# Kernel tuning notes

Hardware: AMD Instinct MI355X
Metric: run time of the kernel (lower is better)

## Reference

```python
import jax, jax.numpy as jnp
import numpy as np
import math

# ---- module config (mirrors init_kwargs) ----
FRAME_H, FRAME_W = 480, 640
HFOV = 79.0
CAM_H_CM = 88.0            # camera_height * 100
NUM_SEM = 16
RES = 5                    # map_resolution (cm/cell)
MAP_SIZE_CM = 4800
DSC = 4                    # global_downscaling
DU = 4                     # du_scale
VR = 100                   # vision_range (cells)
CAT_THR, EXP_THR, MAP_THR = 5.0, 1.0, 1.0
MIN_D_CM, MAX_D_CM = 50.0, 350.0
NC = 6                     # MC.NON_SEM_CHANNELS
ML = MAP_SIZE_CM // DSC // RES   # 240 local map cells
MG = MAP_SIZE_CM // RES          # 960 global map cells
ZMIN = int(-40 / RES)            # -8
ZB = int(360 / RES) - ZMIN       # 80 z bins
MIN_MAP_H = int(25 / RES - ZMIN)            # 13
MAX_MAP_H = int((CAM_H_CM + 1) / RES - ZMIN)  # 25
BC_R = 200 // RES                # been-close radius (cells)
CENTER_POSE = (ML * RES) / 200.0 # agent start at local map center (m)


def _affine_grid(theta, H, W):
    # theta: (B,2,3); align_corners=True convention
    ys = jnp.linspace(-1.0, 1.0, H)
    xs = jnp.linspace(-1.0, 1.0, W)
    xg, yg = jnp.meshgrid(xs, ys)
    base = jnp.stack([xg, yg, jnp.ones_like(xg)], -1)  # (H,W,3)
    return jnp.einsum('bij,hwj->bhwi', theta, base)    # (B,H,W,2)


def _grid_sample(img, grid):
    # bilinear, align_corners=True, zero padding (matches F.grid_sample)
    B, C, H, W = img.shape
    x = (grid[..., 0] + 1.0) * 0.5 * (W - 1)
    y = (grid[..., 1] + 1.0) * 0.5 * (H - 1)
    x0, y0 = jnp.floor(x), jnp.floor(y)
    flat = img.reshape(B, C, H * W)
    out = jnp.zeros_like(img)
    for dx in (0.0, 1.0):
        for dy in (0.0, 1.0):
            xi, yi = x0 + dx, y0 + dy
            w = (1.0 - jnp.abs(x - xi)) * (1.0 - jnp.abs(y - yi))
            ok = (xi >= 0) & (xi <= W - 1) & (yi >= 0) & (yi <= H - 1)
            idx = (jnp.clip(yi, 0, H - 1).astype(jnp.int32) * W
                   + jnp.clip(xi, 0, W - 1).astype(jnp.int32))
            g = jnp.take_along_axis(flat, jnp.broadcast_to(idx.reshape(B, 1, -1), (B, C, H * W)), axis=2)
            out = out + g.reshape(B, C, H, W) * (w * ok)[:, None]
    return out


def _splat(gx, gy, gz, feat, valid):
    # trilinear scatter-add of per-point features into (VR,VR,ZB) voxel grid
    # gx,gy,gz,valid: (B,P); feat: (B,P,F)
    B, P = gx.shape
    F = feat.shape[-1]
    ncell = VR * VR * ZB
    acc = jnp.zeros((B * ncell, F), feat.dtype)
    base = (jnp.arange(B) * ncell)[:, None]
    x0, y0, z0 = jnp.floor(gx), jnp.floor(gy), jnp.floor(gz)
    for dx in (0.0, 1.0):
        for dy in (0.0, 1.0):
            for dz in (0.0, 1.0):
                xi, yi, zi = x0 + dx, y0 + dy, z0 + dz
                w = (1.0 - jnp.abs(gx - xi)) * (1.0 - jnp.abs(gy - yi)) * (1.0 - jnp.abs(gz - zi))
                ok = valid & (xi >= 0) & (xi < VR) & (yi >= 0) & (yi < VR) & (zi >= 0) & (zi < ZB)
                cell = (yi.astype(jnp.int32) * VR + xi.astype(jnp.int32)) * ZB + zi.astype(jnp.int32)
                idx = jnp.clip(base + cell, 0, B * ncell - 1).reshape(-1)
                upd = (feat * (w * ok.astype(feat.dtype))[..., None]).reshape(B * P, F)
                acc = acc.at[idx].add(upd)
    return acc.reshape(B, VR, VR, ZB, F).transpose(0, 4, 1, 2, 3)  # (B,F,VR,VR,ZB)


def _forward(seq_obs, seq_pose_delta, seq_camera_poses, init_local_map,
             init_global_map, init_local_pose, init_global_pose,
             init_lmb, init_origins, seq_dones, seq_update_global):
    B, T = seq_obs.shape[:2]
    C = NUM_SEM
    f = FRAME_W / (2.0 * math.tan(math.radians(HFOV) / 2.0))
    cx, cy = FRAME_W / 2.0, FRAME_H / 2.0
    xs = ((jnp.arange(0, FRAME_W, DU) - cx) / f).astype(jnp.float32)   # (Ws,)
    zr = ((cy - jnp.arange(0, FRAME_H, DU)) / f).astype(jnp.float32)   # (Hs,)
    # camera tilt (elevation) from extrinsics (identity -> 0)
    elev = jnp.arctan2(seq_camera_poses[:, 2, 1], seq_camera_poses[:, 2, 2])
    ce, se = jnp.cos(elev)[:, None, None], jnp.sin(elev)[:, None, None]
    Hs, Ws = FRAME_H // DU, FRAME_W // DU
    P = Hs * Ws
    row = jnp.arange(ML, dtype=jnp.float32)

    def step(carry, inp):
        local_map, global_map, pose = carry
        obs, pd, done, upd = inp
        done = done.astype(bool)
        upd = upd.astype(bool)
        # episode reset
        local_map = jnp.where(done[:, None, None, None], 0.0, local_map)
        global_map = jnp.where(done[:, None, None, None], 0.0, global_map)
        pose = jnp.where(done[:, None], jnp.array([CENTER_POSE, CENTER_POSE, 0.0], jnp.float32), pose)
        # pose update (get_new_pose_batch, degrees)
        tr = jnp.radians(pose[:, 2])
        nx = pose[:, 0] + pd[:, 0] * jnp.cos(tr) - pd[:, 1] * jnp.sin(tr)
        ny = pose[:, 1] + pd[:, 0] * jnp.sin(tr) + pd[:, 1] * jnp.cos(tr)
        nt = jnp.mod(pose[:, 2] + jnp.degrees(pd[:, 2]) + 180.0, 360.0) - 180.0
        pose = jnp.stack([nx, ny, nt], -1)
        # ---- depth -> egocentric point cloud (cm) ----
        d = obs[:, 3, ::DU, ::DU]                           # (B,Hs,Ws)
        valid = (d >= MIN_D_CM) & (d <= MAX_D_CM)
        lat = d * xs[None, None, :]
        up = d * zr[None, :, None]
        fwd = d * ce + up * se
        hgt = -d * se + up * ce + CAM_H_CM
        gx = (lat / RES + VR / 2.0).reshape(B, P)
        gy = (fwd / RES).reshape(B, P)
        gz = (hgt / RES - ZMIN).reshape(B, P)
        # features: occupancy + avg-pooled semantics (du_scale pooling)
        sem = obs[:, 4:].reshape(B, C, Hs, DU, Ws, DU).mean((3, 5))
        feat = jnp.concatenate([jnp.ones((B, 1, Hs, Ws), obs.dtype), sem], 1)
        feat = feat.reshape(B, 1 + C, P).transpose(0, 2, 1)  # (B,P,F)
        vox = _splat(gx, gy, gz, feat, valid.reshape(B, P))  # (B,F,VR,VR,ZB)
        agent_hp = vox[..., MIN_MAP_H:MAX_MAP_H].sum(-1)
        all_hp = vox.sum(-1)
        fp_map = jnp.clip(agent_hp[:, 0:1] / MAP_THR, 0.0, 1.0)
        fp_exp = jnp.clip(all_hp[:, 0:1] / EXP_THR, 0.0, 1.0)
        sem_pred = jnp.clip(agent_hp[:, 1:] / CAT_THR, 0.0, 1.0)
        agent_view = jnp.zeros((B, NC + C, ML, ML), obs.dtype)
        y1, x1 = ML // 2, ML // 2 - VR // 2
        agent_view = agent_view.at[:, 0:1, y1:y1 + VR, x1:x1 + VR].set(fp_map)
        agent_view = agent_view.at[:, 1:2, y1:y1 + VR, x1:x1 + VR].set(fp_exp)
        agent_view = agent_view.at[:, NC:, y1:y1 + VR, x1:x1 + VR].set(sem_pred)
        # ---- pose transform: rotation then translation grid_sample ----
        th = jnp.radians(90.0 - pose[:, 2])
        stx = -(pose[:, 0] * 100.0 / RES - ML / 2.0) / (ML / 2.0)
        sty = -(pose[:, 1] * 100.0 / RES - ML / 2.0) / (ML / 2.0)
        c, s = jnp.cos(th), jnp.sin(th)
        z0 = jnp.zeros_like(th)
        o1 = jnp.ones_like(th)
        th_rot = jnp.stack([jnp.stack([c, -s, z0], -1), jnp.stack([s, c, z0], -1)], 1)
        th_tr = jnp.stack([jnp.stack([o1, z0, stx], -1), jnp.stack([z0, o1, sty], -1)], 1)
        warped = _grid_sample(_grid_sample(agent_view, _affine_grid(th_rot, ML, ML)),
                              _affine_grid(th_tr, ML, ML))
        # dilate obstacle channel (3x3 ones kernel, 1 iter)
        obst = jax.lax.reduce_window(warped[:, 0:1], -jnp.inf, jax.lax.max,
                                     (1, 1, 3, 3), (1, 1, 1, 1), 'SAME')
        warped = warped.at[:, 0:1].set(obst)
        local_map = jnp.maximum(local_map, warped)
        # current location / visited / been-close disks
        acx, acy = pose[:, 0] * 100.0 / RES, pose[:, 1] * 100.0 / RES
        d2 = ((row[None, None, :] - acx[:, None, None]) ** 2
              + (row[None, :, None] - acy[:, None, None]) ** 2)
        curr = (d2 <= 4.0).astype(local_map.dtype)
        local_map = local_map.at[:, 2].set(curr)
        local_map = local_map.at[:, 3].max(curr)
        local_map = local_map.at[:, 4].max((d2 <= float(BC_R ** 2)).astype(local_map.dtype))
        # global map update at local map boundaries
        gnew = jax.vmap(lambda g, l, lm: jax.lax.dynamic_update_slice(g, l, (0, lm[0], lm[2])))(
            global_map, local_map, init_lmb)
        global_map = jnp.where(upd[:, None, None, None], gnew, global_map)
        gpose = pose + init_origins
        # map features: local NC ch + maxpooled global NC ch + local sem ch
        gmax = global_map[:, :NC].reshape(B, NC, MG // DSC, DSC, MG // DSC, DSC).max((3, 5))
        mf = jnp.concatenate([local_map[:, :NC], gmax, local_map[:, NC:]], 1)
        return (local_map, global_map, pose), (mf, pose, gpose)

    xs_t = (jnp.swapaxes(seq_obs, 0, 1), jnp.swapaxes(seq_pose_delta, 0, 1),
            jnp.swapaxes(seq_dones, 0, 1), jnp.swapaxes(seq_update_global, 0, 1))
    (fl, fg, _), (mfs, lps, gps) = jax.lax.scan(
        step, (init_local_map, init_global_map, init_local_pose), xs_t)
    seq_mf = jnp.swapaxes(mfs, 0, 1)
    seq_lp = jnp.swapaxes(lps, 0, 1)
    seq_gp = jnp.swapaxes(gps, 0, 1)
    seq_lmb = jnp.broadcast_to(init_lmb[:, None], (B, T, 4))
    seq_org = jnp.broadcast_to(init_origins[:, None], (B, T, 3))
    return seq_mf, fl, fg, seq_lp, seq_gp, seq_lmb, seq_org


def setup_inputs():
    key = jax.random.key(0)
    k0, k1 = jax.random.split(key)
    B, T = 4, 4
    obs = jax.random.uniform(k0, (B, T, 4 + NUM_SEM, FRAME_H, FRAME_W), jnp.float32)
    obs = obs.at[:, :, 3].set(MIN_D_CM + obs[:, :, 3] * (MAX_D_CM - MIN_D_CM))  # depth in cm
    obs = obs.at[:, :, 4:].set((obs[:, :, 4:] > 0.9).astype(jnp.float32))       # binary seg masks
    pd = jax.random.normal(k1, (B, T, 3), jnp.float32) * jnp.array([0.25, 0.05, 0.1], jnp.float32)
    lo = (MG - ML) // 2
    lmb = jnp.tile(jnp.array([[lo, lo + ML, lo, lo + ML]], jnp.int32), (B, 1))
    origins = jnp.concatenate([jnp.full((B, 2), lo * RES / 100.0, jnp.float32),
                               jnp.zeros((B, 1), jnp.float32)], 1)
    lp = jnp.concatenate([jnp.full((B, 2), CENTER_POSE, jnp.float32),
                          jnp.zeros((B, 1), jnp.float32)], 1)
    return {
        "seq_obs": obs,
        "seq_pose_delta": pd,
        "seq_camera_poses": jnp.broadcast_to(jnp.eye(4, dtype=jnp.float32), (B, 4, 4)),
        "init_local_map": jnp.zeros((B, NC + NUM_SEM, ML, ML), jnp.float32),
        "init_global_map": jnp.zeros((B, NC + NUM_SEM, MG, MG), jnp.float32),
        "init_local_pose": lp,
        "init_global_pose": lp + origins,
        "init_origins": origins,
        "seq_dones": jnp.zeros((B, T), jnp.int32),
        "seq_update_global": jnp.ones((B, T), jnp.int32),
        "init_lmb": lmb,
    }


def reference(seq_obs, seq_pose_delta, seq_camera_poses, init_local_map, init_global_map,
              init_local_pose, init_global_pose, init_origins, seq_dones,
              seq_update_global, init_lmb):
    return _forward(seq_obs, seq_pose_delta, seq_camera_poses, init_local_map,
                    init_global_map, init_local_pose, init_global_pose,
                    init_lmb, init_origins, seq_dones, seq_update_global)
```

## Files before the change

kernel.cpp:

```cpp
#include <hip/hip_runtime.h>
#include <math.h>

#ifndef M_PI
#define M_PI 3.14159265358979323846
#endif

#define BB 4
#define TT 4
#define NSEM 16
#define CHL 22
#define CHMF 28
#define ML 240
#define MG 960
#define VR 100
#define HS 120
#define WSW 160
#define NPL 18
#define CPAD 24
#define MLSQ (ML*ML)
#define MGSQ (MG*MG)
#define VRSQ (VR*VR)
#define PPT (HS*WSW)
#define NPART 12
#define PR 9
#define NGRP 5

#define SZ_MF (BB*TT*CHMF*MLSQ)
#define SZ_FL (BB*CHL*MLSQ)
#define SZ_FG (BB*CHL*MGSQ)
#define OFF_FL SZ_MF
#define OFF_FG (OFF_FL + SZ_FL)
#define OFF_LP (OFF_FG + SZ_FG)
#define OFF_GP (OFF_LP + BB*TT*3)
#define OFF_LMB (OFF_GP + BB*TT*3)
#define OFF_ORG (OFF_LMB + BB*TT*4)

#define WS_SCAL 0
#define WS_FLAGS (WS_SCAL + BB*TT*8)
#define WS_CACHE (WS_FLAGS + 4*BB)
#define WS_PLANES (WS_CACHE + BB*6*MLSQ)
#define WS_I2 (WS_PLANES + BB*TT*VRSQ*CPAD)
#define PTSN (BB*TT*PPT)
#define WS_GY (WS_I2 + BB*TT*NPL*MLSQ)
#define WS_GX (WS_GY + PTSN)
#define WS_WZA (WS_GX + PTSN)
#define WS_WZL (WS_WZA + PTSN)
#define WS_SEMDS (WS_WZL + PTSN)

__global__ __launch_bounds__(256) void k_stage1(const float* __restrict__ obs,
                                                const float* __restrict__ cam,
                                                const float* __restrict__ pd,
                                                const float* __restrict__ ilp,
                                                const float* __restrict__ org,
                                                const int* __restrict__ lmb,
                                                const int* __restrict__ dones,
                                                const int* __restrict__ updg,
                                                float* __restrict__ out,
                                                float* __restrict__ ws)
{
    if (blockIdx.x == 0) {
        int i = threadIdx.x;
        if (i < BB*TT) {
            int b = i / TT, t = i % TT;
            for (int k = 0; k < 4; k++) out[OFF_LMB + (b*TT+t)*4 + k] = (float)lmb[b*4+k];
            for (int k = 0; k < 3; k++) out[OFF_ORG + (b*TT+t)*3 + k] = org[b*3+k];
        }
        if (i >= BB) return;
        int b = i;
        float p0 = ilp[b*3+0], p1 = ilp[b*3+1], p2 = ilp[b*3+2];
        const float D2R = 0.017453292519943295f;
        int lastDone = -1, lastUpd = -1;
        for (int t = 0; t < TT; t++) {
            if (dones[b*TT+t]) { p0 = 6.0f; p1 = 6.0f; p2 = 0.0f; lastDone = t; }
            if (updg[b*TT+t]) lastUpd = t;
            float tr = p2 * D2R;
            float c0 = cosf(tr), s0 = sinf(tr);
            float q0 = pd[(b*TT+t)*3+0], q1 = pd[(b*TT+t)*3+1], q2 = pd[(b*TT+t)*3+2];
            float nx = p0 + q0*c0 - q1*s0;
            float ny = p1 + q0*s0 + q1*c0;
            float a  = p2 + q2*57.29577951308232f + 180.0f;
            float m  = fmodf(a, 360.0f); if (m < 0.0f) m += 360.0f;
            float nt = m - 180.0f;
            p0 = nx; p1 = ny; p2 = nt;
            out[OFF_LP + (b*TT+t)*3+0] = nx;
            out[OFF_LP + (b*TT+t)*3+1] = ny;
            out[OFF_LP + (b*TT+t)*3+2] = nt;
            out[OFF_GP + (b*TT+t)*3+0] = nx + org[b*3+0];
            out[OFF_GP + (b*TT+t)*3+1] = ny + org[b*3+1];
            out[OFF_GP + (b*TT+t)*3+2] = nt + org[b*3+2];
            float th = (90.0f - nt) * D2R;
            float ax = nx*100.0f/5.0f, ay = ny*100.0f/5.0f;
            float* sc = ws + WS_SCAL + (b*TT+t)*8;
            sc[0] = cosf(th);
            sc[1] = sinf(th);
            sc[2] = -(ax - 120.0f)/120.0f;
            sc[3] = -(ay - 120.0f)/120.0f;
            sc[4] = ax;
            sc[5] = ay;
        }
        ws[WS_FLAGS + b*4 + 0] = (lastDone >= 0) ? 1.0f : 0.0f;
        ws[WS_FLAGS + b*4 + 1] = (lastUpd < lastDone) ? 1.0f : 0.0f;
        ws[WS_FLAGS + b*4 + 2] = (float)lastUpd;
        return;
    }
    int bb = blockIdx.x - 1;
    int bt = bb / 75;
    int b = bt / TT;
    int p = (bb % 75)*256 + threadIdx.x;
    int h = p / WSW, w = p % WSW;
    size_t pi = (size_t)bt*PPT + p;
    const float* ob = obs + (size_t)bt * 20 * 480 * 640;
    float d = ob[(size_t)(3*480 + 4*h)*640 + 4*w];
    if (!(d >= 50.0f && d <= 350.0f)) { ws[WS_GY + pi] = -1000.0f; return; }

    double fd = 640.0 / (2.0 * tan((79.0 * M_PI / 180.0) * 0.5));
    float ff  = (float)fd;
    float xsv = (float)(4*w - 320) / ff;
    float zrv = (240.0f - (float)(4*h)) / ff;
    float elev = atan2f(cam[b*16+9], cam[b*16+10]);
    float ce = cosf(elev), se = sinf(elev);
    float up  = d * zrv;
    float fwd = d*ce + up*se;
    float hgt = -d*se + up*ce + 88.0f;
    float gx = (d*xsv)/5.0f + 50.0f;
    float gy = fwd/5.0f;
    float gz = hgt/5.0f + 8.0f;

    float z0 = floorf(gz);
    float wza = 0.0f, wzl = 0.0f;
    #pragma unroll
    for (int dz = 0; dz < 2; dz++) {
        float zi = z0 + dz;
        float wz = 1.0f - fabsf(gz - zi);
        if (zi >= 0.0f && zi < 80.0f) {
            wzl += wz;
            if (zi >= 13.0f && zi < 25.0f) wza += wz;
        }
    }
    if (wzl == 0.0f && wza == 0.0f) { ws[WS_GY + pi] = -1000.0f; return; }

    ws[WS_GY + pi]  = gy;
    ws[WS_GX + pi]  = gx;
    ws[WS_WZA + pi] = wza;
    ws[WS_WZL + pi] = wzl;

    if (wza > 0.0f) {
        const float* sb = ob + (size_t)4*480*640 + (size_t)(4*h)*640 + 4*w;
        float* so = ws + WS_SEMDS + (size_t)bt*NSEM*PPT + p;
        #pragma unroll
        for (int k = 0; k < NSEM; k++) {
            float s = 0.0f;
            #pragma unroll
            for (int r = 0; r < 4; r++) {
                const float4 v = *(const float4*)(sb + (size_t)k*480*640 + r*640);
                s += v.x + v.y + v.z + v.w;
            }
            so[(size_t)k*PPT] = s * 0.0625f;
        }
    }
}

__global__ __launch_bounds__(256) void k_splat2(const float* __restrict__ ws,
                                                float* __restrict__ planes)
{
    int bt = blockIdx.x;
    int part = blockIdx.y;
    int grp = blockIdx.z;
    int rlo = part * PR;
    int c0  = (grp == 0) ? 0 : (2 + 4*(grp-1));
    int nch = (grp == 0) ? 2 : 4;
    __shared__ float acc[4*PR*VR];
    for (int e = threadIdx.x; e < nch*PR*VR; e += 256) acc[e] = 0.0f;
    __syncthreads();

    const float* gyA  = ws + WS_GY  + (size_t)bt*PPT;
    const float* gxA  = ws + WS_GX  + (size_t)bt*PPT;
    const float* wzaA = ws + WS_WZA + (size_t)bt*PPT;
    const float* wzlA = ws + WS_WZL + (size_t)bt*PPT;
    const float* semA = ws + WS_SEMDS + (size_t)bt*NSEM*PPT + (size_t)(c0-2)*PPT;

    for (int p = threadIdx.x; p < PPT; p += 256) {
        float gy = gyA[p];
        float y0 = floorf(gy);
        if (y0 > (float)(rlo + PR - 1) || y0 + 1.0f < (float)rlo) continue;
        float wza = wzaA[p];
        if (grp != 0 && wza <= 0.0f) continue;
        float gx  = gxA[p];
        float x0 = floorf(gx);
        float sem[4];
        if (grp != 0) {
            #pragma unroll
            for (int k = 0; k < 4; k++) sem[k] = semA[(size_t)k*PPT + p];
        }
        float wzl = (grp == 0) ? wzlA[p] : 0.0f;
        #pragma unroll
        for (int dy = 0; dy < 2; dy++) {
            float yi = y0 + dy;
            if (!(yi >= 0.0f && yi < 100.0f)) continue;
            int r = (int)yi - rlo;
            if (r < 0 || r >= PR) continue;
            float wy = 1.0f - fabsf(gy - yi);
            #pragma unroll
            for (int dx = 0; dx < 2; dx++) {
                float xi = x0 + dx;
                if (!(xi >= 0.0f && xi < 100.0f)) continue;
                float wxy = (1.0f - fabsf(gx - xi)) * wy;
                if (wxy <= 0.0f) continue;
                int cell = r*VR + (int)xi;
                if (grp == 0) {
                    if (wza > 0.0f) atomicAdd(&acc[cell], wza*wxy);
                    if (wzl > 0.0f) atomicAdd(&acc[PR*VR + cell], wzl*wxy);
                } else {
                    #pragma unroll
                    for (int k = 0; k < 4; k++) {
                        float sv = sem[k];
                        if (sv != 0.0f) atomicAdd(&acc[k*PR*VR + cell], sv*wza*wxy);
                    }
                }
            }
        }
    }
    __syncthreads();

    int nrows = 100 - rlo; if (nrows > PR) nrows = PR;
    if (nrows <= 0) return;
    float* pl = planes + (size_t)bt*VRSQ*CPAD;
    for (int e = threadIdx.x; e < nch*nrows*VR; e += 256) {
        int c = e / (nrows*VR);
        int rc = e % (nrows*VR);
        int r = rc / VR, x = rc % VR;
        pl[(size_t)((rlo + r)*VR + x)*CPAD + (c0 + c)] = acc[c*PR*VR + r*VR + x];
    }
}

__global__ __launch_bounds__(256) void k_stage3(const float* __restrict__ planes,
                                                const float* __restrict__ igm,
                                                const int* __restrict__ dones,
                                                const int* __restrict__ lmb,
                                                float* __restrict__ I2,
                                                float* __restrict__ fg,
                                                float* __restrict__ out,
                                                float* __restrict__ ws)
{
    int bid = blockIdx.x;
    if (bid < 3600) {
        int bt = bid / 225;
        int idx = (bid % 225)*256 + threadIdx.x;
        int i = idx / ML, j = idx % ML;
        const float* sc = ws + WS_SCAL + bt*8;
        float c = sc[0], s = sc[1], stx = sc[2], sty = sc[3];
        float* o = I2 + (size_t)bt*NPL*MLSQ + idx;
        const float* pl = planes + (size_t)bt*VRSQ*CPAD;

        int   soff[16];
        float sw[16];
        float wsum = 0.0f;
        {
            float xg = (float)j * (float)(2.0/239.0) - 1.0f + stx;
            float yg = (float)i * (float)(2.0/239.0) - 1.0f + sty;
            float x = (xg + 1.0f)*0.5f*239.0f;
            float y = (yg + 1.0f)*0.5f*239.0f;
            float x0 = floorf(x), y0 = floorf(y);
            #pragma unroll
            for (int dy = 0; dy < 2; dy++) {
                float yi = y0 + dy;
                bool vy = (yi >= 0.0f && yi <= 239.0f);
                float wy = 1.0f - fabsf(y - yi);
                #pragma unroll
                for (int dx = 0; dx < 2; dx++) {
                    float xi = x0 + dx;
                    bool vx = (xi >= 0.0f && xi <= 239.0f);
                    float w2v = (vy && vx) ? (1.0f - fabsf(x - xi)) * wy : 0.0f;
                    int ci = (dy*2 + dx)*4;
                    float xg1 = (float)(int)xi * (float)(2.0/239.0) - 1.0f;
                    float yg1 = (float)(int)yi * (float)(2.0/239.0) - 1.0f;
                    float gxr = c*xg1 - s*yg1;
                    float gyr = s*xg1 + c*yg1;
                    float xx = (gxr + 1.0f)*0.5f*239.0f;
                    float yy = (gyr + 1.0f)*0.5f*239.0f;
                    float xx0 = floorf(xx), yy0 = floorf(yy);
                    #pragma unroll
                    for (int dy1 = 0; dy1 < 2; dy1++) {
                        float syi = yy0 + dy1;
                        bool v1y = (syi >= 120.0f && syi < 220.0f);
                        float wy1 = 1.0f - fabsf(yy - syi);
                        #pragma unroll
                        for (int dx1 = 0; dx1 < 2; dx1++) {
                            float sxi = xx0 + dx1;
                            bool v1 = v1y && (sxi >= 70.0f && sxi < 170.0f);
                            float w1v = v1 ? (1.0f - fabsf(xx - sxi)) * wy1 : 0.0f;
                            float wt = w2v * w1v;
                            soff[ci + dy1*2 + dx1] = v1 ? ((int)syi - 120)*VR + ((int)sxi - 70) : 0;
                            sw[ci + dy1*2 + dx1] = wt;
                            wsum += wt;
                        }
                    }
                }
            }
        }

        if (wsum <= 0.0f) {
            #pragma unroll
            for (int cc = 0; cc < NPL; cc++) o[(size_t)cc*MLSQ] = 0.0f;
            return;
        }
        float acc[NPL];
        #pragma unroll
        for (int cc = 0; cc < NPL; cc++) acc[cc] = 0.0f;
        #pragma unroll
        for (int k = 0; k < 16; k++) {
            float w = sw[k];
            if (w == 0.0f) continue;
            const float* pb = pl + (size_t)soff[k]*CPAD;
            float4 a0 = *(const float4*)(pb + 0);
            float4 a1 = *(const float4*)(pb + 4);
            float4 a2 = *(const float4*)(pb + 8);
            float4 a3 = *(const float4*)(pb + 12);
            float2 a4 = *(const float2*)(pb + 16);
            acc[0]  += fminf(a0.x, 1.0f) * w;
            acc[1]  += fminf(a0.y, 1.0f) * w;
            acc[2]  += fminf(a0.z / 5.0f, 1.0f) * w;
            acc[3]  += fminf(a0.w / 5.0f, 1.0f) * w;
            acc[4]  += fminf(a1.x / 5.0f, 1.0f) * w;
            acc[5]  += fminf(a1.y / 5.0f, 1.0f) * w;
            acc[6]  += fminf(a1.z / 5.0f, 1.0f) * w;
            acc[7]  += fminf(a1.w / 5.0f, 1.0f) * w;
            acc[8]  += fminf(a2.x / 5.0f, 1.0f) * w;
            acc[9]  += fminf(a2.y / 5.0f, 1.0f) * w;
            acc[10] += fminf(a2.z / 5.0f, 1.0f) * w;
            acc[11] += fminf(a2.w / 5.0f, 1.0f) * w;
            acc[12] += fminf(a3.x / 5.0f, 1.0f) * w;
            acc[13] += fminf(a3.y / 5.0f, 1.0f) * w;
            acc[14] += fminf(a3.z / 5.0f, 1.0f) * w;
            acc[15] += fminf(a3.w / 5.0f, 1.0f) * w;
            acc[16] += fminf(a4.x / 5.0f, 1.0f) * w;
            acc[17] += fminf(a4.y / 5.0f, 1.0f) * w;
        }
        #pragma unroll
        for (int cc = 0; cc < NPL; cc++) o[(size_t)cc*MLSQ] = acc[cc];
        return;
    }
    int fb = bid - 3600;
    int blk = fb % 225;
    int c = (fb / 225) % CHL;
    int b = fb / (225*CHL);
    int idx = blk*256 + threadIdx.x;
    int i = idx / ML, j = idx % ML;
    bool anyDone = ws[WS_FLAGS + b*4 + 0] > 0.5f;
    bool zeroWin = ws[WS_FLAGS + b*4 + 1] > 0.5f;
    int lastUpd  = (int)ws[WS_FLAGS + b*4 + 2];
    int y0 = lmb[b*4+0], x0 = lmb[b*4+2];
    int iy0 = y0 >> 2, ix0 = x0 >> 2;
    bool inWin = (i >= iy0) && (i < iy0 + ML/4) && (j >= ix0) && (j < ix0 + ML/4);

    size_t base = ((size_t)b*CHL + c)*MGSQ + (size_t)(4*i)*MG + 4*j;
    const float* g = igm + base;
    float* go = fg + base;

    int act;
    if (inWin) act = zeroWin ? 1 : ((lastUpd >= 0) ? 2 : (anyDone ? 1 : 0));
    else       act = anyDone ? 1 : 0;

    if (c < 6) {
        float m = -3.0e38f;
        #pragma unroll
        for (int r = 0; r < 4; r++) {
            float4 q = *(const float4*)(g + (size_t)r*MG);
            if (act == 0) *(float4*)(go + (size_t)r*MG) = q;
            else if (act == 1) *(float4*)(go + (size_t)r*MG) = make_float4(0,0,0,0);
            m = fmaxf(m, fmaxf(fmaxf(q.x, q.y), fmaxf(q.z, q.w)));
        }
        ws[WS_CACHE + ((size_t)b*6 + c)*MLSQ + idx] = m;
        if (!inWin) {
            float v = m;
            for (int t = 0; t < TT; t++) {
                if (dones[b*TT+t]) v = 0.0f;
                out[(size_t)(b*TT+t)*CHMF*MLSQ + (6+c)*MLSQ + idx] = v;
            }
        }
    } else {
        if (act == 2) return;
        if (act == 1) {
            float4 z = make_float4(0,0,0,0);
            #pragma unroll
            for (int r = 0; r < 4; r++) *(float4*)(go + (size_t)r*MG) = z;
        } else {
            #pragma unroll
            for (int r = 0; r < 4; r++)
                *(float4*)(go + (size_t)r*MG) = *(const float4*)(g + (size_t)r*MG);
        }
    }
}

__global__ __launch_bounds__(256) void k_updl7(const float* __restrict__ I2,
                                               const float* __restrict__ ws,
                                               const float* __restrict__ ilm,
                                               const int* __restrict__ dones,
                                               const int* __restrict__ updg,
                                               const int* __restrict__ lmb,
                                               float* __restrict__ fl,
                                               float* __restrict__ fg,
                                               float* __restrict__ out)
{
    int bz = blockIdx.z;
    int b = bz / 7, g = bz % 7;
    int gi = blockIdx.y;
    int bx = blockIdx.x;
    int lane = threadIdx.x & 63, wv = threadIdx.x >> 6;
    int j0 = (bx < 3) ? bx*64 : 176;
    int j = j0 + lane;
    int i = gi*4 + wv;
    int idx = i*ML + j;

    int ncl, cl[4];
    switch (g) {
        case 0:  ncl = 1; cl[0] = 0; cl[1] = 0; cl[2] = 0; cl[3] = 0; break;
        case 1:  ncl = 3; cl[0] = 1; cl[1] = 2; cl[2] = 3; cl[3] = 0; break;
        case 2:  ncl = 2; cl[0] = 4; cl[1] = 5; cl[2] = 0; cl[3] = 0; break;
        default: ncl = 4; { int cc0 = 6 + (g-3)*4;
                 cl[0] = cc0; cl[1] = cc0+1; cl[2] = cc0+2; cl[3] = cc0+3; } break;
    }
    bool hasG = (g <= 2);

    __shared__ float red[4][3][16];

    const float* lmsrc = ilm + (size_t)b*CHL*MLSQ;
    float* lm = fl + (size_t)b*CHL*MLSQ;
    int y0 = lmb[b*4+0], x0 = lmb[b*4+2];
    bool zeroWin = ws[WS_FLAGS + b*4 + 1] > 0.5f;
    int lastUpd = (int)ws[WS_FLAGS + b*4 + 2];

    float S[4];
    #pragma unroll
    for (int q = 0; q < 4; q++) {
        int c = cl[q];
        S[q] = (q < ncl && c != 2) ? lmsrc[c*MLSQ + idx] : 0.0f;
    }

    bool writer = hasG && (wv == 0) && ((lane & 3) == 0);
    int cx = lane >> 2;
    int cellY = (y0 >> 2) + gi;
    int cellX = (x0 >> 2) + (j0 >> 2) + cx;
    float W[3];
    if (writer) {
        #pragma unroll
        for (int q = 0; q < 3; q++)
            if (q < ncl)
                W[q] = ws[WS_CACHE + ((size_t)b*6 + cl[q])*MLSQ + cellY*ML + cellX];
    }

    for (int t = 0; t < TT; t++) {
        int bt = b*TT + t;
        bool done = dones[bt] != 0;
        bool upd  = updg[bt] != 0;
        const float* src = I2 + (size_t)bt*NPL*MLSQ;
        float* mf = out + (size_t)bt*CHMF*MLSQ;

        float pooled = -3.0e38f;
        if (g == 0) {
            for (int di = -1; di <= 1; di++) {
                int ii = i + di; if (ii < 0 || ii >= ML) continue;
                for (int dj = -1; dj <= 1; dj++) {
                    int jj = j + dj; if (jj < 0 || jj >= ML) continue;
                    pooled = fmaxf(pooled, src[ii*ML + jj]);
                }
            }
        }
        const float* sc = ws + WS_SCAL + bt*8;
        float acx = sc[4], acy = sc[5];
        float ddx = (float)j - acx, ddy = (float)i - acy;
        float d2 = ddx*ddx + ddy*ddy;
        float curr = (d2 <= 4.0f) ? 1.0f : 0.0f;
        float bc   = (d2 <= 1600.0f) ? 1.0f : 0.0f;

        size_t goff = (size_t)(y0+i)*MG + (x0+j);
        bool wrG = (t == lastUpd) && !zeroWin;

        #pragma unroll
        for (int q = 0; q < 4; q++) {
            if (q >= ncl) continue;
            int c = cl[q];
            if (done) S[q] = 0.0f;
            float nv;
            if      (c == 0) nv = fmaxf(S[q], pooled);
            else if (c == 1) nv = fmaxf(S[q], src[MLSQ + idx]);
            else if (c == 2) nv = curr;
            else if (c == 3) nv = fmaxf(S[q], curr);
            else if (c == 4) nv = fmaxf(S[q], bc);
            else if (c == 5) nv = S[q];
            else             nv = fmaxf(S[q], src[(size_t)(c-4)*MLSQ + idx]);
            S[q] = nv;
            mf[(size_t)(c < 6 ? c : c + 6)*MLSQ + idx] = nv;
            if (wrG) fg[((size_t)b*CHL + c)*MGSQ + goff] = nv;
        }

        if (hasG) {
            #pragma unroll
            for (int q = 0; q < 3; q++) {
                if (q >= ncl) continue;
                float v = S[q];
                v = fmaxf(v, __shfl_xor(v, 1, 64));
                v = fmaxf(v, __shfl_xor(v, 2, 64));
                if ((lane & 3) == 0) red[wv][q][cx] = v;
            }
            __syncthreads();
            if (writer) {
                #pragma unroll
                for (int q = 0; q < 3; q++) {
                    if (q >= ncl) continue;
                    if (done) W[q] = 0.0f;
                    if (upd)  W[q] = fmaxf(fmaxf(red[0][q][cx], red[1][q][cx]),
                                           fmaxf(red[2][q][cx], red[3][q][cx]));
                    mf[(size_t)(6 + cl[q])*MLSQ + cellY*ML + cellX] = W[q];
                }
            }
            __syncthreads();
        }
    }
    #pragma unroll
    for (int q = 0; q < 4; q++)
        if (q < ncl) lm[(size_t)cl[q]*MLSQ + idx] = S[q];
}

extern "C" void kernel_launch(void* const* d_in, const int* in_sizes, int n_in,
                              void* d_out, int out_size, void* d_ws, size_t ws_size,
                              hipStream_t stream)
{
    const float* obs   = (const float*)d_in[0];
    const float* pd    = (const float*)d_in[1];
    const float* cam   = (const float*)d_in[2];
    const float* ilm   = (const float*)d_in[3];
    const float* igm   = (const float*)d_in[4];
    const float* ilp   = (const float*)d_in[5];
    const float* org   = (const float*)d_in[7];
    const int*   dones = (const int*)d_in[8];
    const int*   updg  = (const int*)d_in[9];
    const int*   lmb   = (const int*)d_in[10];
    float* out = (float*)d_out;
    float* ws  = (float*)d_ws;

    float* fl     = out + OFF_FL;
    float* fg     = out + OFF_FG;
    float* planes = ws + WS_PLANES;
    float* I2v    = ws + WS_I2;

    k_stage1<<<1 + 75*BB*TT, 256, 0, stream>>>(obs, cam, pd, ilp, org, lmb,
                                               dones, updg, out, ws);
    k_splat2<<<dim3(BB*TT, NPART, NGRP), 256, 0, stream>>>(ws, planes);
    k_stage3<<<3600 + 225*CHL*BB, 256, 0, stream>>>(planes, igm, dones, lmb,
                                                    I2v, fg, out, ws);
    k_updl7<<<dim3(4, 60, BB*7), 256, 0, stream>>>(I2v, ws, ilm, dones, updg, lmb,
                                                   fl, fg, out);
}
```

Measured before the change: 358.4 us.

## Spread global-map init work across the first three kernels to overlap stages

The global-map initialisation (downsample max, copy or zero of 22 channels) used to run entirely in the third kernel. It is now split across the first three kernels: channels 0-5 alongside the point projection, 6-13 alongside the splat, and 14-21 alongside the plane processing. Each piece computes its done/update flags locally instead of reading them from the workspace. The aim is to fill idle CUs during the small projection and splat launches with bandwidth-heavy copy work, at the cost of larger grids and mixed block types in each kernel.

```diff
diff --git a/kernel.cpp b/kernel.cpp
--- a/kernel.cpp
+++ b/kernel.cpp
@@ -24,6 +24,7 @@
 #define NPART 12
 #define PR 9
 #define NGRP 5
+#define NSPLAT (BB*TT*NPART*NGRP)
 
 #define SZ_MF (BB*TT*CHMF*MLSQ)
 #define SZ_FL (BB*CHL*MLSQ)
@@ -47,16 +48,79 @@
 #define WS_WZL (WS_WZA + PTSN)
 #define WS_SEMDS (WS_WZL + PTSN)
 
-__global__ __launch_bounds__(256) void k_stage1(const float* __restrict__ obs,
-                                                const float* __restrict__ cam,
-                                                const float* __restrict__ pd,
-                                                const float* __restrict__ ilp,
-                                                const float* __restrict__ org,
-                                                const int* __restrict__ lmb,
-                                                const int* __restrict__ dones,
-                                                const int* __restrict__ updg,
-                                                float* __restrict__ out,
-                                                float* __restrict__ ws)
+__device__ __forceinline__ void fginit_block(const float* __restrict__ igm,
+                                             const int* __restrict__ dones,
+                                             const int* __restrict__ updg,
+                                             const int* __restrict__ lmb,
+                                             float* __restrict__ fg,
+                                             float* __restrict__ out,
+                                             float* __restrict__ ws,
+                                             int b, int c, int idx)
+{
+    int i = idx / ML, j = idx % ML;
+    int lastDone = -1, lastUpd = -1;
+    #pragma unroll
+    for (int t = 0; t < TT; t++) {
+        if (dones[b*TT+t]) lastDone = t;
+        if (updg[b*TT+t])  lastUpd  = t;
+    }
+    bool anyDone = lastDone >= 0;
+    bool zeroWin = lastUpd < lastDone;
+    int y0 = lmb[b*4+0], x0 = lmb[b*4+2];
+    int iy0 = y0 >> 2, ix0 = x0 >> 2;
+    bool inWin = (i >= iy0) && (i < iy0 + ML/4) && (j >= ix0) && (j < ix0 + ML/4);
+
+    size_t base = ((size_t)b*CHL + c)*MGSQ + (size_t)(4*i)*MG + 4*j;
+    const float* g = igm + base;
+    float* go = fg + base;
+
+    int act;
+    if (inWin) act = zeroWin ? 1 : ((lastUpd >= 0) ? 2 : (anyDone ? 1 : 0));
+    else       act = anyDone ? 1 : 0;
+
+    if (c < 6) {
+        float m = -3.0e38f;
+        #pragma unroll
+        for (int r = 0; r < 4; r++) {
+            float4 q = *(const float4*)(g + (size_t)r*MG);
+            if (act == 0) *(float4*)(go + (size_t)r*MG) = q;
+            else if (act == 1) *(float4*)(go + (size_t)r*MG) = make_float4(0,0,0,0);
+            m = fmaxf(m, fmaxf(fmaxf(q.x, q.y), fmaxf(q.z, q.w)));
+        }
+        ws[WS_CACHE + ((size_t)b*6 + c)*MLSQ + idx] = m;
+        if (!inWin) {
+            float v = m;
+            for (int t = 0; t < TT; t++) {
+                if (dones[b*TT+t]) v = 0.0f;
+                out[(size_t)(b*TT+t)*CHMF*MLSQ + (6+c)*MLSQ + idx] = v;
+            }
+        }
+    } else {
+        if (act == 2) return;
+        if (act == 1) {
+            float4 z = make_float4(0,0,0,0);
+            #pragma unroll
+            for (int r = 0; r < 4; r++) *(float4*)(go + (size_t)r*MG) = z;
+        } else {
+            #pragma unroll
+            for (int r = 0; r < 4; r++)
+                *(float4*)(go + (size_t)r*MG) = *(const float4*)(g + (size_t)r*MG);
+        }
+    }
+}
+
+__global__ __launch_bounds__(256) void k_node1(const float* __restrict__ obs,
+                                               const float* __restrict__ cam,
+                                               const float* __restrict__ pd,
+                                               const float* __restrict__ ilp,
+                                               const float* __restrict__ org,
+                                               const int* __restrict__ lmb,
+                                               const int* __restrict__ dones,
+                                               const int* __restrict__ updg,
+                                               const float* __restrict__ igm,
+                                               float* __restrict__ fg,
+                                               float* __restrict__ out,
+                                               float* __restrict__ ws)
 {
     if (blockIdx.x == 0) {
         int i = threadIdx.x;
@@ -103,144 +167,168 @@
         ws[WS_FLAGS + b*4 + 2] = (float)lastUpd;
         return;
     }
-    int bb = blockIdx.x - 1;
-    int bt = bb / 75;
-    int b = bt / TT;
-    int p = (bb % 75)*256 + threadIdx.x;
-    int h = p / WSW, w = p % WSW;
-    size_t pi = (size_t)bt*PPT + p;
-    const float* ob = obs + (size_t)bt * 20 * 480 * 640;
-    float d = ob[(size_t)(3*480 + 4*h)*640 + 4*w];
-    if (!(d >= 50.0f && d <= 350.0f)) { ws[WS_GY + pi] = -1000.0f; return; }
-
-    double fd = 640.0 / (2.0 * tan((79.0 * M_PI / 180.0) * 0.5));
-    float ff  = (float)fd;
-    float xsv = (float)(4*w - 320) / ff;
-    float zrv = (240.0f - (float)(4*h)) / ff;
-    float elev = atan2f(cam[b*16+9], cam[b*16+10]);
-    float ce = cosf(elev), se = sinf(elev);
-    float up  = d * zrv;
-    float fwd = d*ce + up*se;
-    float hgt = -d*se + up*ce + 88.0f;
-    float gx = (d*xsv)/5.0f + 50.0f;
-    float gy = fwd/5.0f;
-    float gz = hgt/5.0f + 8.0f;
-
-    float z0 = floorf(gz);
-    float wza = 0.0f, wzl = 0.0f;
-    #pragma unroll
-    for (int dz = 0; dz < 2; dz++) {
-        float zi = z0 + dz;
-        float wz = 1.0f - fabsf(gz - zi);
-        if (zi >= 0.0f && zi < 80.0f) {
-            wzl += wz;
-            if (zi >= 13.0f && zi < 25.0f) wza += wz;
-        }
-    }
-    if (wzl == 0.0f && wza == 0.0f) { ws[WS_GY + pi] = -1000.0f; return; }
-
-    ws[WS_GY + pi]  = gy;
-    ws[WS_GX + pi]  = gx;
-    ws[WS_WZA + pi] = wza;
-    ws[WS_WZL + pi] = wzl;
-
-    if (wza > 0.0f) {
-        const float* sb = ob + (size_t)4*480*640 + (size_t)(4*h)*640 + 4*w;
-        float* so = ws + WS_SEMDS + (size_t)bt*NSEM*PPT + p;
-        #pragma unroll
-        for (int k = 0; k < NSEM; k++) {
-            float s = 0.0f;
-            #pragma unroll
-            for (int r = 0; r < 4; r++) {
-                const float4 v = *(const float4*)(sb + (size_t)k*480*640 + r*640);
-                s += v.x + v.y + v.z + v.w;
-            }
-            so[(size_t)k*PPT] = s * 0.0625f;
-        }
-    }
+    if (blockIdx.x <= 75*BB*TT) {
+        int bb = blockIdx.x - 1;
+        int bt = bb / 75;
+        int b = bt / TT;
+        int p = (bb % 75)*256 + threadIdx.x;
+        int h = p / WSW, w = p % WSW;
+        size_t pi = (size_t)bt*PPT + p;
+        const float* ob = obs + (size_t)bt * 20 * 480 * 640;
+        float d = ob[(size_t)(3*480 + 4*h)*640 + 4*w];
+        if (!(d >= 50.0f && d <= 350.0f)) { ws[WS_GY + pi] = -1000.0f; return; }
+
+        double fd = 640.0 / (2.0 * tan((79.0 * M_PI / 180.0) * 0.5));
+        float ff  = (float)fd;
+        float xsv = (float)(4*w - 320) / ff;
+        float zrv = (240.0f - (float)(4*h)) / ff;
+        float elev = atan2f(cam[b*16+9], cam[b*16+10]);
+        float ce = cosf(elev), se = sinf(elev);
+        float up  = d * zrv;
+        float fwd = d*ce + up*se;
+        float hgt = -d*se + up*ce + 88.0f;
+        float gx = (d*xsv)/5.0f + 50.0f;
+        float gy = fwd/5.0f;
+        float gz = hgt/5.0f + 8.0f;
+
+        float z0 = floorf(gz);
+        float wza = 0.0f, wzl = 0.0f;
+        #pragma unroll
+        for (int dz = 0; dz < 2; dz++) {
+            float zi = z0 + dz;
+            float wz = 1.0f - fabsf(gz - zi);
+            if (zi >= 0.0f && zi < 80.0f) {
+                wzl += wz;
+                if (zi >= 13.0f && zi < 25.0f) wza += wz;
+            }
+        }
+        if (wzl == 0.0f && wza == 0.0f) { ws[WS_GY + pi] = -1000.0f; return; }
+
+        ws[WS_GY + pi]  = gy;
+        ws[WS_GX + pi]  = gx;
+        ws[WS_WZA + pi] = wza;
+        ws[WS_WZL + pi] = wzl;
+
+        if (wza > 0.0f) {
+            const float* sb = ob + (size_t)4*480*640 + (size_t)(4*h)*640 + 4*w;
+            float* so = ws + WS_SEMDS + (size_t)bt*NSEM*PPT + p;
+            #pragma unroll
+            for (int k = 0; k < NSEM; k++) {
+                float s = 0.0f;
+                #pragma unroll
+                for (int r = 0; r < 4; r++) {
+                    const float4 v = *(const float4*)(sb + (size_t)k*480*640 + r*640);
+                    s += v.x + v.y + v.z + v.w;
+                }
+                so[(size_t)k*PPT] = s * 0.0625f;
+            }
+        }
+        return;
+    }
+    int fb = blockIdx.x - (1 + 75*BB*TT);
+    int idx = (fb % 225)*256 + threadIdx.x;
+    int c = (fb / 225) % 6;
+    int b = fb / (225*6);
+    fginit_block(igm, dones, updg, lmb, fg, out, ws, b, c, idx);
 }
 
-__global__ __launch_bounds__(256) void k_splat2(const float* __restrict__ ws,
-                                                float* __restrict__ planes)
+__global__ __launch_bounds__(256) void k_node2(const float* __restrict__ igm,
+                                               const int* __restrict__ dones,
+                                               const int* __restrict__ updg,
+                                               const int* __restrict__ lmb,
+                                               float* __restrict__ planes,
+                                               float* __restrict__ fg,
+                                               float* __restrict__ out,
+                                               float* __restrict__ ws)
 {
-    int bt = blockIdx.x;
-    int part = blockIdx.y;
-    int grp = blockIdx.z;
-    int rlo = part * PR;
-    int c0  = (grp == 0) ? 0 : (2 + 4*(grp-1));
-    int nch = (grp == 0) ? 2 : 4;
     __shared__ float acc[4*PR*VR];
-    for (int e = threadIdx.x; e < nch*PR*VR; e += 256) acc[e] = 0.0f;
-    __syncthreads();
-
-    const float* gyA  = ws + WS_GY  + (size_t)bt*PPT;
-    const float* gxA  = ws + WS_GX  + (size_t)bt*PPT;
-    const float* wzaA = ws + WS_WZA + (size_t)bt*PPT;
-    const float* wzlA = ws + WS_WZL + (size_t)bt*PPT;
-    const float* semA = ws + WS_SEMDS + (size_t)bt*NSEM*PPT + (size_t)(c0-2)*PPT;
-
-    for (int p = threadIdx.x; p < PPT; p += 256) {
-        float gy = gyA[p];
-        float y0 = floorf(gy);
-        if (y0 > (float)(rlo + PR - 1) || y0 + 1.0f < (float)rlo) continue;
-        float wza = wzaA[p];
-        if (grp != 0 && wza <= 0.0f) continue;
-        float gx  = gxA[p];
-        float x0 = floorf(gx);
-        float sem[4];
-        if (grp != 0) {
-            #pragma unroll
-            for (int k = 0; k < 4; k++) sem[k] = semA[(size_t)k*PPT + p];
-        }
-        float wzl = (grp == 0) ? wzlA[p] : 0.0f;
-        #pragma unroll
-        for (int dy = 0; dy < 2; dy++) {
-            float yi = y0 + dy;
-            if (!(yi >= 0.0f && yi < 100.0f)) continue;
-            int r = (int)yi - rlo;
-            if (r < 0 || r >= PR) continue;
-            float wy = 1.0f - fabsf(gy - yi);
-            #pragma unroll
-            for (int dx = 0; dx < 2; dx++) {
-                float xi = x0 + dx;
-                if (!(xi >= 0.0f && xi < 100.0f)) continue;
-                float wxy = (1.0f - fabsf(gx - xi)) * wy;
-                if (wxy <= 0.0f) continue;
-                int cell = r*VR + (int)xi;
-                if (grp == 0) {
-                    if (wza > 0.0f) atomicAdd(&acc[cell], wza*wxy);
-                    if (wzl > 0.0f) atomicAdd(&acc[PR*VR + cell], wzl*wxy);
-                } else {
-                    #pragma unroll
-                    for (int k = 0; k < 4; k++) {
-                        float sv = sem[k];
-                        if (sv != 0.0f) atomicAdd(&acc[k*PR*VR + cell], sv*wza*wxy);
+    int bid = blockIdx.x;
+    if (bid < NSPLAT) {
+        int bt = bid & 15;
+        int part = (bid >> 4) % NPART;
+        int grp = bid / (16*NPART);
+        int rlo = part * PR;
+        int c0  = (grp == 0) ? 0 : (2 + 4*(grp-1));
+        int nch = (grp == 0) ? 2 : 4;
+        for (int e = threadIdx.x; e < nch*PR*VR; e += 256) acc[e] = 0.0f;
+        __syncthreads();
+
+        const float* gyA  = ws + WS_GY  + (size_t)bt*PPT;
+        const float* gxA  = ws + WS_GX  + (size_t)bt*PPT;
+        const float* wzaA = ws + WS_WZA + (size_t)bt*PPT;
+        const float* wzlA = ws + WS_WZL + (size_t)bt*PPT;
+        const float* semA = ws + WS_SEMDS + (size_t)bt*NSEM*PPT + (size_t)(c0-2)*PPT;
+
+        for (int p = threadIdx.x; p < PPT; p += 256) {
+            float gy = gyA[p];
+            float y0 = floorf(gy);
+            if (y0 > (float)(rlo + PR - 1) || y0 + 1.0f < (float)rlo) continue;
+            float wza = wzaA[p];
+            if (grp != 0 && wza <= 0.0f) continue;
+            float gx  = gxA[p];
+            float x0 = floorf(gx);
+            float sem[4];
+            if (grp != 0) {
+                #pragma unroll
+                for (int k = 0; k < 4; k++) sem[k] = semA[(size_t)k*PPT + p];
+            }
+            float wzl = (grp == 0) ? wzlA[p] : 0.0f;
+            #pragma unroll
+            for (int dy = 0; dy < 2; dy++) {
+                float yi = y0 + dy;
+                if (!(yi >= 0.0f && yi < 100.0f)) continue;
+                int r = (int)yi - rlo;
+                if (r < 0 || r >= PR) continue;
+                float wy = 1.0f - fabsf(gy - yi);
+                #pragma unroll
+                for (int dx = 0; dx < 2; dx++) {
+                    float xi = x0 + dx;
+                    if (!(xi >= 0.0f && xi < 100.0f)) continue;
+                    float wxy = (1.0f - fabsf(gx - xi)) * wy;
+                    if (wxy <= 0.0f) continue;
+                    int cell = r*VR + (int)xi;
+                    if (grp == 0) {
+                        if (wza > 0.0f) atomicAdd(&acc[cell], wza*wxy);
+                        if (wzl > 0.0f) atomicAdd(&acc[PR*VR + cell], wzl*wxy);
+                    } else {
+                        #pragma unroll
+                        for (int k = 0; k < 4; k++) {
+                            float sv = sem[k];
+                            if (sv != 0.0f) atomicAdd(&acc[k*PR*VR + cell], sv*wza*wxy);
+                        }
                     }
                 }
             }
         }
-    }
-    __syncthreads();
-
-    int nrows = 100 - rlo; if (nrows > PR) nrows = PR;
-    if (nrows <= 0) return;
-    float* pl = planes + (size_t)bt*VRSQ*CPAD;
-    for (int e = threadIdx.x; e < nch*nrows*VR; e += 256) {
-        int c = e / (nrows*VR);
-        int rc = e % (nrows*VR);
-        int r = rc / VR, x = rc % VR;
-        pl[(size_t)((rlo + r)*VR + x)*CPAD + (c0 + c)] = acc[c*PR*VR + r*VR + x];
-    }
+        __syncthreads();
+
+        int nrows = 100 - rlo; if (nrows > PR) nrows = PR;
+        if (nrows <= 0) return;
+        float* pl = planes + (size_t)bt*VRSQ*CPAD;
+        for (int e = threadIdx.x; e < nch*nrows*VR; e += 256) {
+            int c = e / (nrows*VR);
+            int rc = e % (nrows*VR);
+            int r = rc / VR, x = rc % VR;
+            pl[(size_t)((rlo + r)*VR + x)*CPAD + (c0 + c)] = acc[c*PR*VR + r*VR + x];
+        }
+        return;
+    }
+    int fb = bid - NSPLAT;
+    int idx = (fb % 225)*256 + threadIdx.x;
+    int c = 6 + (fb / 225) % 8;
+    int b = fb / (225*8);
+    fginit_block(igm, dones, updg, lmb, fg, out, ws, b, c, idx);
 }
 
-__global__ __launch_bounds__(256) void k_stage3(const float* __restrict__ planes,
-                                                const float* __restrict__ igm,
-                                                const int* __restrict__ dones,
-                                                const int* __restrict__ lmb,
-                                                float* __restrict__ I2,
-                                                float* __restrict__ fg,
-                                                float* __restrict__ out,
-                                                float* __restrict__ ws)
+__global__ __launch_bounds__(256) void k_node3(const float* __restrict__ planes,
+                                               const float* __restrict__ igm,
+                                               const int* __restrict__ dones,
+                                               const int* __restrict__ updg,
+                                               const int* __restrict__ lmb,
+                                               float* __restrict__ I2,
+                                               float* __restrict__ fg,
+                                               float* __restrict__ out,
+                                               float* __restrict__ ws)
 {
     int bid = blockIdx.x;
     if (bid < 3600) {
@@ -341,55 +429,10 @@
         return;
     }
     int fb = bid - 3600;
-    int blk = fb % 225;
-    int c = (fb / 225) % CHL;
-    int b = fb / (225*CHL);
-    int idx = blk*256 + threadIdx.x;
-    int i = idx / ML, j = idx % ML;
-    bool anyDone = ws[WS_FLAGS + b*4 + 0] > 0.5f;
-    bool zeroWin = ws[WS_FLAGS + b*4 + 1] > 0.5f;
-    int lastUpd  = (int)ws[WS_FLAGS + b*4 + 2];
-    int y0 = lmb[b*4+0], x0 = lmb[b*4+2];
-    int iy0 = y0 >> 2, ix0 = x0 >> 2;
-    bool inWin = (i >= iy0) && (i < iy0 + ML/4) && (j >= ix0) && (j < ix0 + ML/4);
-
-    size_t base = ((size_t)b*CHL + c)*MGSQ + (size_t)(4*i)*MG + 4*j;
-    const float* g = igm + base;
-    float* go = fg + base;
-
-    int act;
-    if (inWin) act = zeroWin ? 1 : ((lastUpd >= 0) ? 2 : (anyDone ? 1 : 0));
-    else       act = anyDone ? 1 : 0;
-
-    if (c < 6) {
-        float m = -3.0e38f;
-        #pragma unroll
-        for (int r = 0; r < 4; r++) {
-            float4 q = *(const float4*)(g + (size_t)r*MG);
-            if (act == 0) *(float4*)(go + (size_t)r*MG) = q;
-            else if (act == 1) *(float4*)(go + (size_t)r*MG) = make_float4(0,0,0,0);
-            m = fmaxf(m, fmaxf(fmaxf(q.x, q.y), fmaxf(q.z, q.w)));
-        }
-        ws[WS_CACHE + ((size_t)b*6 + c)*MLSQ + idx] = m;
-        if (!inWin) {
-            float v = m;
-            for (int t = 0; t < TT; t++) {
-                if (dones[b*TT+t]) v = 0.0f;
-                out[(size_t)(b*TT+t)*CHMF*MLSQ + (6+c)*MLSQ + idx] = v;
-            }
-        }
-    } else {
-        if (act == 2) return;
-        if (act == 1) {
-            float4 z = make_float4(0,0,0,0);
-            #pragma unroll
-            for (int r = 0; r < 4; r++) *(float4*)(go + (size_t)r*MG) = z;
-        } else {
-            #pragma unroll
-            for (int r = 0; r < 4; r++)
-                *(float4*)(go + (size_t)r*MG) = *(const float4*)(g + (size_t)r*MG);
-        }
-    }
+    int idx = (fb % 225)*256 + threadIdx.x;
+    int c = 14 + (fb / 225) % 8;
+    int b = fb / (225*8);
+    fginit_block(igm, dones, updg, lmb, fg, out, ws, b, c, idx);
 }
 
 __global__ __launch_bounds__(256) void k_updl7(const float* __restrict__ I2,
@@ -544,11 +587,12 @@
     float* planes = ws + WS_PLANES;
     float* I2v    = ws + WS_I2;
 
-    k_stage1<<<1 + 75*BB*TT, 256, 0, stream>>>(obs, cam, pd, ilp, org, lmb,
-                                               dones, updg, out, ws);
-    k_splat2<<<dim3(BB*TT, NPART, NGRP), 256, 0, stream>>>(ws, planes);
-    k_stage3<<<3600 + 225*CHL*BB, 256, 0, stream>>>(planes, igm, dones, lmb,
-                                                    I2v, fg, out, ws);
+    k_node1<<<1 + 75*BB*TT + 225*6*BB, 256, 0, stream>>>(obs, cam, pd, ilp, org, lmb,
+                                                         dones, updg, igm, fg, out, ws);
+    k_node2<<<NSPLAT + 225*8*BB, 256, 0, stream>>>(igm, dones, updg, lmb,
+                                                   planes, fg, out, ws);
+    k_node3<<<3600 + 225*8*BB, 256, 0, stream>>>(planes, igm, dones, updg, lmb,
+                                                 I2v, fg, out, ws);
     k_updl7<<<dim3(4, 60, BB*7), 256, 0, stream>>>(I2v, ws, ilm, dones, updg, lmb,
                                                    fl, fg, out);
 }
```

Measured after the change: 370.4 us. 1.03x slower.
